# Performance work log

Measured on AMD Instinct MI355X. Metric: run time of the kernel, lower is better.

## Reference

```python
import jax, jax.numpy as jnp
import numpy as np


def setup_inputs() -> dict:
    key = jax.random.key(0)
    k1, = jax.random.split(key, 1)
    num_bins = 5
    x = jax.random.uniform(k1, (16, 3, 1024, 1024), dtype=jnp.float32)
    widths = jnp.ones((num_bins,), jnp.float32) / num_bins
    heights = jnp.linspace(0.0, 1.0, num_bins + 1, dtype=jnp.float32)
    slopes = jnp.ones((num_bins + 1,), jnp.float32)
    return {"x": x, "widths": widths, "heights": heights, "slopes": slopes}


def reference(x, widths, heights, slopes):
    num_bins = widths.shape[0]
    original_shape = x.shape
    xf = jnp.clip(x.reshape(-1), 0.0, 1.0)
    bin_edges = jnp.cumsum(widths)                       # [num_bins]
    bin_idx = jnp.searchsorted(bin_edges, xf)            # side='left' matches torch default
    bin_idx = jnp.clip(bin_idx, 0, num_bins - 1)
    widths_cumsum = jnp.concatenate([jnp.zeros((1,), widths.dtype), bin_edges[:-1]])
    x_low = widths_cumsum[bin_idx]
    x_high = (widths_cumsum + widths)[bin_idx]
    y_low = heights[:-1][bin_idx]
    y_high = heights[1:][bin_idx]
    slope_low = slopes[:-1][bin_idx]
    slope_high = slopes[1:][bin_idx]
    t = (xf - x_low) / (x_high - x_low + 1e-8)
    numerator = slope_low * t ** 2 + 2.0 * t * (1.0 - t)
    s = slope_low + slope_high
    denominator = s * t ** 2 + 2.0 * (s - 2.0) * t + 2.0
    y = y_low + (y_high - y_low) * numerator / denominator
    return y.reshape(original_shape)
```

## Files before the change

kernel.cpp:

```cpp
#include <hip/hip_runtime.h>

#define NBINS 5

__global__ __launch_bounds__(256) void ToneMapping_kernel(
    const float* __restrict__ x,
    const float* __restrict__ widths,
    const float* __restrict__ heights,
    const float* __restrict__ slopes,
    float* __restrict__ out,
    long long n4, long long n)
{
    __shared__ float s_edge[NBINS - 1];
    __shared__ float s_xl[NBINS];
    __shared__ float s_iw[NBINS];
    __shared__ float s_yl[NBINS];
    __shared__ float s_dy[NBINS];
    __shared__ float s_slm2[NBINS];
    __shared__ float s_s[NBINS];
    __shared__ float s_s2m4[NBINS];

    if (threadIdx.x == 0) {
        float edges[NBINS], wc[NBINS];
        float c = 0.0f;
        for (int i = 0; i < NBINS; ++i) {
            wc[i] = c;
            c = c + widths[i];
            edges[i] = c;
        }
        for (int i = 0; i < NBINS; ++i) {
            float xl = wc[i];
            float xh = wc[i] + widths[i];
            s_xl[i] = xl;
            s_iw[i] = 1.0f / (xh - xl + 1e-8f);
            float yl = heights[i], yh = heights[i + 1];
            s_yl[i] = yl;
            s_dy[i] = yh - yl;
            float sl = slopes[i], sh = slopes[i + 1];
            s_slm2[i] = sl - 2.0f;
            float ss = sl + sh;
            s_s[i]    = ss;
            s_s2m4[i] = 2.0f * (ss - 2.0f);
            if (i < NBINS - 1) s_edge[i] = edges[i];
        }
    }
    __syncthreads();

    long long tid    = (long long)blockIdx.x * blockDim.x + threadIdx.x;
    long long stride = (long long)gridDim.x * blockDim.x;

    const float4* __restrict__ x4 = (const float4*)x;
    float4* __restrict__ o4 = (float4*)out;

    for (long long i = tid; i < n4; i += stride) {
        float4 v = x4[i];
        float in[4]  = {v.x, v.y, v.z, v.w};
        float res[4];
        #pragma unroll
        for (int k = 0; k < 4; ++k) {
            float xf = fminf(fmaxf(in[k], 0.0f), 1.0f);
            int idx = 0;
            #pragma unroll
            for (int j = 0; j < NBINS - 1; ++j)
                idx += (s_edge[j] < xf) ? 1 : 0;

            float t  = (xf - s_xl[idx]) * s_iw[idx];
            float t2 = t * t;
            float num = fmaf(t2, s_slm2[idx], 2.0f * t);
            float den = fmaf(s_s[idx], t2, fmaf(s_s2m4[idx], t, 2.0f));
            float r   = __builtin_amdgcn_rcpf(den);
            res[k] = fmaf(s_dy[idx], num * r, s_yl[idx]);
        }
        o4[i] = make_float4(res[0], res[1], res[2], res[3]);
    }

    long long tail_start = n4 * 4;
    for (long long i = tail_start + tid; i < n; i += stride) {
        float xf = fminf(fmaxf(x[i], 0.0f), 1.0f);
        int idx = 0;
        for (int j = 0; j < NBINS - 1; ++j) idx += (s_edge[j] < xf) ? 1 : 0;
        float t  = (xf - s_xl[idx]) * s_iw[idx];
        float t2 = t * t;
        float num = fmaf(t2, s_slm2[idx], 2.0f * t);
        float den = fmaf(s_s[idx], t2, fmaf(s_s2m4[idx], t, 2.0f));
        out[i] = fmaf(s_dy[idx], num * __builtin_amdgcn_rcpf(den), s_yl[idx]);
    }
}

extern "C" void kernel_launch(void* const* d_in, const int* in_sizes, int n_in,
                              void* d_out, int out_size, void* d_ws, size_t ws_size,
                              hipStream_t stream) {
    const float* x       = (const float*)d_in[0];
    const float* widths  = (const float*)d_in[1];
    const float* heights = (const float*)d_in[2];
    const float* slopes  = (const float*)d_in[3];
    float* out = (float*)d_out;

    long long n  = (long long)in_sizes[0];
    long long n4 = n / 4;

    const int block = 256;
    long long want = (n4 + block - 1) / block;
    int grid = (int)(want < 2048 ? (want > 0 ? want : 1) : 2048);

    ToneMapping_kernel<<<grid, block, 0, stream>>>(x, widths, heights, slopes, out, n4, n);
}
```

Measured before the change: 79.79 us.

## Pack bin parameters into float4 LDS, unroll grid-stride loop, use nontemporal memory ops

Per-bin coefficients are packed into two float4 shared arrays so each element needs two vector LDS reads instead of seven scalar ones. The bin edges are hoisted into registers. The main loop now issues four independent 16-byte nontemporal loads per iteration before computing, and writes with nontemporal stores. The aim is more memory-level parallelism and less streaming-cache pollution in a bandwidth-bound kernel, at the cost of higher register use.

```diff
diff --git a/kernel.cpp b/kernel.cpp
--- a/kernel.cpp
+++ b/kernel.cpp
@@ -1,6 +1,8 @@
 #include <hip/hip_runtime.h>
 
 #define NBINS 5
+
+typedef float f32x4 __attribute__((ext_vector_type(4)));
 
 __global__ __launch_bounds__(256) void ToneMapping_kernel(
     const float* __restrict__ x,
@@ -10,79 +12,84 @@
     float* __restrict__ out,
     long long n4, long long n)
 {
-    __shared__ float s_edge[NBINS - 1];
-    __shared__ float s_xl[NBINS];
-    __shared__ float s_iw[NBINS];
-    __shared__ float s_yl[NBINS];
-    __shared__ float s_dy[NBINS];
-    __shared__ float s_slm2[NBINS];
-    __shared__ float s_s[NBINS];
-    __shared__ float s_s2m4[NBINS];
+    __shared__ float4 s_pA[NBINS];
+    __shared__ float4 s_pB[NBINS];
+    __shared__ float  s_edge[NBINS - 1];
 
     if (threadIdx.x == 0) {
-        float edges[NBINS], wc[NBINS];
         float c = 0.0f;
         for (int i = 0; i < NBINS; ++i) {
-            wc[i] = c;
-            c = c + widths[i];
-            edges[i] = c;
-        }
-        for (int i = 0; i < NBINS; ++i) {
-            float xl = wc[i];
-            float xh = wc[i] + widths[i];
-            s_xl[i] = xl;
-            s_iw[i] = 1.0f / (xh - xl + 1e-8f);
+            float w  = widths[i];
+            float xl = c;
+            c = c + w;
+            if (i < NBINS - 1) s_edge[i] = c;
+            float xh = xl + w;
             float yl = heights[i], yh = heights[i + 1];
-            s_yl[i] = yl;
-            s_dy[i] = yh - yl;
-            float sl = slopes[i], sh = slopes[i + 1];
-            s_slm2[i] = sl - 2.0f;
+            float sl = slopes[i],  sh = slopes[i + 1];
             float ss = sl + sh;
-            s_s[i]    = ss;
-            s_s2m4[i] = 2.0f * (ss - 2.0f);
-            if (i < NBINS - 1) s_edge[i] = edges[i];
+            s_pA[i] = make_float4(xl, 1.0f / (xh - xl + 1e-8f), yl, yh - yl);
+            s_pB[i] = make_float4(sl - 2.0f, ss, 2.0f * (ss - 2.0f), 0.0f);
         }
     }
     __syncthreads();
 
+    float e0 = s_edge[0], e1 = s_edge[1], e2 = s_edge[2], e3 = s_edge[3];
+
     long long tid    = (long long)blockIdx.x * blockDim.x + threadIdx.x;
     long long stride = (long long)gridDim.x * blockDim.x;
 
-    const float4* __restrict__ x4 = (const float4*)x;
-    float4* __restrict__ o4 = (float4*)out;
+    const f32x4* __restrict__ x4 = (const f32x4*)x;
+    f32x4* __restrict__ o4 = (f32x4*)out;
 
-    for (long long i = tid; i < n4; i += stride) {
-        float4 v = x4[i];
-        float in[4]  = {v.x, v.y, v.z, v.w};
-        float res[4];
+    auto evalv = [&](f32x4 v) -> f32x4 {
+        f32x4 r;
         #pragma unroll
         for (int k = 0; k < 4; ++k) {
-            float xf = fminf(fmaxf(in[k], 0.0f), 1.0f);
-            int idx = 0;
-            #pragma unroll
-            for (int j = 0; j < NBINS - 1; ++j)
-                idx += (s_edge[j] < xf) ? 1 : 0;
+            float xf = fminf(fmaxf(v[k], 0.0f), 1.0f);
+            int idx = (int)(e0 < xf) + (int)(e1 < xf) + (int)(e2 < xf) + (int)(e3 < xf);
+            float4 pA = s_pA[idx];
+            float4 pB = s_pB[idx];
+            float t   = (xf - pA.x) * pA.y;
+            float t2  = t * t;
+            float num = fmaf(t2, pB.x, t + t);
+            float den = fmaf(pB.y, t2, fmaf(pB.z, t, 2.0f));
+            r[k] = fmaf(pA.w, num * __builtin_amdgcn_rcpf(den), pA.z);
+        }
+        return r;
+    };
 
-            float t  = (xf - s_xl[idx]) * s_iw[idx];
-            float t2 = t * t;
-            float num = fmaf(t2, s_slm2[idx], 2.0f * t);
-            float den = fmaf(s_s[idx], t2, fmaf(s_s2m4[idx], t, 2.0f));
-            float r   = __builtin_amdgcn_rcpf(den);
-            res[k] = fmaf(s_dy[idx], num * r, s_yl[idx]);
-        }
-        o4[i] = make_float4(res[0], res[1], res[2], res[3]);
+    long long i = tid;
+    const long long step4 = 4 * stride;
+    for (; i + 3 * stride < n4; i += step4) {
+        f32x4 v0 = __builtin_nontemporal_load(x4 + i);
+        f32x4 v1 = __builtin_nontemporal_load(x4 + i + stride);
+        f32x4 v2 = __builtin_nontemporal_load(x4 + i + 2 * stride);
+        f32x4 v3 = __builtin_nontemporal_load(x4 + i + 3 * stride);
+        f32x4 r0 = evalv(v0);
+        f32x4 r1 = evalv(v1);
+        f32x4 r2 = evalv(v2);
+        f32x4 r3 = evalv(v3);
+        __builtin_nontemporal_store(r0, o4 + i);
+        __builtin_nontemporal_store(r1, o4 + i + stride);
+        __builtin_nontemporal_store(r2, o4 + i + 2 * stride);
+        __builtin_nontemporal_store(r3, o4 + i + 3 * stride);
+    }
+    for (; i < n4; i += stride) {
+        f32x4 v = __builtin_nontemporal_load(x4 + i);
+        __builtin_nontemporal_store(evalv(v), o4 + i);
     }
 
-    long long tail_start = n4 * 4;
-    for (long long i = tail_start + tid; i < n; i += stride) {
-        float xf = fminf(fmaxf(x[i], 0.0f), 1.0f);
-        int idx = 0;
-        for (int j = 0; j < NBINS - 1; ++j) idx += (s_edge[j] < xf) ? 1 : 0;
-        float t  = (xf - s_xl[idx]) * s_iw[idx];
-        float t2 = t * t;
-        float num = fmaf(t2, s_slm2[idx], 2.0f * t);
-        float den = fmaf(s_s[idx], t2, fmaf(s_s2m4[idx], t, 2.0f));
-        out[i] = fmaf(s_dy[idx], num * __builtin_amdgcn_rcpf(den), s_yl[idx]);
+    long long ts = n4 * 4;
+    for (long long j = ts + tid; j < n; j += stride) {
+        float xf = fminf(fmaxf(x[j], 0.0f), 1.0f);
+        int idx = (int)(e0 < xf) + (int)(e1 < xf) + (int)(e2 < xf) + (int)(e3 < xf);
+        float4 pA = s_pA[idx];
+        float4 pB = s_pB[idx];
+        float t   = (xf - pA.x) * pA.y;
+        float t2  = t * t;
+        float num = fmaf(t2, pB.x, t + t);
+        float den = fmaf(pB.y, t2, fmaf(pB.z, t, 2.0f));
+        out[j] = fmaf(pA.w, num * __builtin_amdgcn_rcpf(den), pA.z);
     }
 }
 
```

New measurement: 85.71 us. 7.4% more time.
